# Kernel optimization log

Measured on AMD Instinct MI355X. Metric: run time of the kernel, lower is better.

Reference implementation:

```python
import jax, jax.numpy as jnp
import numpy as np

H = W = 200
A = 9
N = H * W * A  # 360000 anchors
PRE_NMS = 6000   # test mode
POST_NMS = 300
MIN_SIZE = 16.0 / 1000.0
IOU_THR = 0.7


def _conv(x, w, b, pad):
    y = jax.lax.conv_general_dilated(x, w, (1, 1), pad,
                                     dimension_numbers=("NCHW", "OIHW", "NCHW"))
    return y + b[None, :, None, None]


def _nms_keep(boxes, valid, thr):
    # boxes: [PRE_NMS,4] sorted by descending score; valid: [PRE_NMS] bool
    x1, y1, x2, y2 = boxes[:, 0], boxes[:, 1], boxes[:, 2], boxes[:, 3]
    areas = (x2 - x1) * (y2 - y1)
    idx = jnp.arange(boxes.shape[0])

    def body(i, keep):
        xx1 = jnp.maximum(x1[i], x1)
        yy1 = jnp.maximum(y1[i], y1)
        xx2 = jnp.minimum(x2[i], x2)
        yy2 = jnp.minimum(y2[i], y2)
        inter = jnp.clip(xx2 - xx1, 0.0) * jnp.clip(yy2 - yy1, 0.0)
        iou = inter / (areas[i] + areas - inter + 1e-12)
        suppress = (iou > thr) & (idx > i) & keep[i]
        return keep & ~suppress

    return jax.lax.fori_loop(0, boxes.shape[0], body, valid)


def setup_inputs():
    key = jax.random.key(0)
    ks = jax.random.split(key, 6)
    features = jax.random.normal(ks[0], (1, 512, H, W), dtype=jnp.float32)
    # valid anchor boxes (xyxy, normalized)
    c = jax.random.uniform(ks[1], (N, 2), dtype=jnp.float32)
    wh = jax.random.uniform(ks[2], (N, 2), dtype=jnp.float32, minval=0.02, maxval=0.4)
    anchor = jnp.clip(jnp.concatenate([c - wh / 2, c + wh / 2], axis=1), 0.0, 1.0)
    w1 = 0.01 * jax.random.normal(ks[3], (512, 512, 3, 3), dtype=jnp.float32)
    b1 = jnp.zeros((512,), jnp.float32)
    wc = 0.01 * jax.random.normal(ks[4], (2 * A, 512, 1, 1), dtype=jnp.float32)
    bc = jnp.zeros((2 * A,), jnp.float32)
    wl = 0.01 * jax.random.normal(ks[5], (4 * A, 512, 1, 1), dtype=jnp.float32)
    bl = jnp.zeros((4 * A,), jnp.float32)
    return {"features": features, "anchor": anchor,
            "w1": w1, "b1": b1, "wc": wc, "bc": bc, "wl": wl, "bl": bl}


def reference(features, anchor, w1, b1, wc, bc, wl, bl):
    x = jax.nn.relu(_conv(features, w1, b1, ((1, 1), (1, 1))))
    pred_cls = _conv(x, wc, bc, ((0, 0), (0, 0)))
    pred_loc = _conv(x, wl, bl, ((0, 0), (0, 0)))
    pred_cls = jnp.transpose(pred_cls, (0, 2, 3, 1)).reshape(1, -1, 2)  # [1,N,2]
    pred_loc = jnp.transpose(pred_loc, (0, 2, 3, 1)).reshape(1, -1, 4)  # [1,N,4]

    loc = pred_loc[0]
    cls = pred_cls[0]
    # xy_to_cxcy
    a_cxcy = jnp.concatenate([(anchor[:, 2:] + anchor[:, :2]) / 2.0,
                              anchor[:, 2:] - anchor[:, :2]], axis=1)
    # decode
    cxcy = loc[:, :2] * a_cxcy[:, 2:] + a_cxcy[:, :2]
    wh = jnp.exp(loc[:, 2:]) * a_cxcy[:, 2:]
    # cxcy_to_xy + clamp
    roi = jnp.clip(jnp.concatenate([cxcy - wh / 2.0, cxcy + wh / 2.0], axis=1), 0.0, 1.0)

    scores = jax.nn.softmax(cls, axis=-1)[:, 1]
    ws = roi[:, 2] - roi[:, 0]
    hs = roi[:, 3] - roi[:, 1]
    valid = (hs >= MIN_SIZE) & (ws >= MIN_SIZE)
    scores = jnp.where(valid, scores, -1.0)  # filtered boxes sort last

    top_scores, top_idx = jax.lax.top_k(scores, PRE_NMS)
    boxes = roi[top_idx]                      # [PRE_NMS,4]
    valid_top = top_scores >= 0.0

    keep = jax.lax.stop_gradient(_nms_keep(boxes, valid_top, IOU_THR))
    # first POST_NMS kept boxes, in score order; pad with zeros (fixed shape)
    priority = jnp.where(keep, jnp.arange(PRE_NMS), PRE_NMS)
    order = jnp.argsort(priority)[:POST_NMS]
    rois = jnp.where((priority[order] < PRE_NMS)[:, None], boxes[order], 0.0)  # [300,4]
    return pred_cls, pred_loc, rois
```

## Files before the change

kernel.cpp:

```cpp
#include <hip/hip_runtime.h>

typedef unsigned long long u64;
typedef unsigned int u32;
typedef unsigned short ushort_t;

#define HH 200
#define WW 200
#define HWP 40000
#define NANCH 360000
#define PRE 6000
#define POST 300
#define NW 94
#define NBINS 16384
#define KCAP 8192
#define CS 40

typedef __attribute__((ext_vector_type(8))) _Float16 f16x8;
typedef __attribute__((ext_vector_type(4))) float f32x4;

static constexpr size_t X_F    = 0;
static constexpr size_t X_CNT  = 512ULL*HWP + 64;
static constexpr size_t W1B_F  = X_F + X_CNT;
static constexpr size_t WT64_F = W1B_F + 4608ULL*512;
static constexpr size_t B64_F  = WT64_F + 512ULL*64;
static constexpr size_t SC_F   = B64_F + 64;
static constexpr size_t ROI_F  = SC_F + NANCH;
static constexpr size_t BOX_F  = ROI_F + 4ULL*NANCH;
static constexpr size_t FEND_F = BOX_F + 6016ULL*4;
static constexpr size_t HIST_B = ((FEND_F*4 + 255)/256)*256;
static constexpr size_t CTRL_B = HIST_B + NBINS*4;
static constexpr size_t KEY_B  = CTRL_B + 256;
static constexpr size_t SORT_B = KEY_B + (size_t)KCAP*8;
static constexpr size_t VALW_B = SORT_B + 6016ULL*8;
static constexpr size_t MASK_B = ((VALW_B + NW*8 + 255)/256)*256;
static constexpr size_t WS_END = MASK_B + (size_t)PRE*NW*8;

__device__ __forceinline__ u32 fsort(float f) {
  u32 u = __float_as_uint(f);
  return (u & 0x80000000u) ? ~u : (u | 0x80000000u);
}
__device__ __forceinline__ int bucket_of(float s) {
  int b = (int)((s + 1.0f) * 8191.0f);
  return b < 0 ? 0 : (b > 16383 ? 16383 : b);
}
__device__ __forceinline__ ushort_t h_bits(_Float16 h) {
  union { _Float16 h; ushort_t u; } c; c.h = h; return c.u;
}
__device__ __forceinline__ void split_pack(float fA, float fB, u32& w1, u32& w2) {
  _Float16 hA = (_Float16)fA, hB = (_Float16)fB;
  float rA = fA - (float)hA, rB = fB - (float)hB;
  _Float16 cA = (_Float16)(rA * 2048.0f), cB = (_Float16)(rB * 2048.0f);
  w1 = (u32)h_bits(hA) | ((u32)h_bits(hB) << 16);
  w2 = (u32)h_bits(cA) | ((u32)h_bits(cB) << 16);
}

__global__ void pack_w1b(const float* __restrict__ w1, ushort_t* __restrict__ p12) {
  int idx = blockIdx.x*256 + threadIdx.x;
  if (idx >= 512*4608) return;
  int och = idx / 4608, k = idx - (idx/4608)*4608;
  float f = w1[idx];
  _Float16 h1 = (_Float16)f;
  float r = f - (float)h1;
  _Float16 h2 = (_Float16)(r * 2048.0f);
  int ci = k / 9, tap = k - ci*9;
  int chunk = ci >> 5, cil = ci & 31;
  int s = chunk*9 + tap;
  int z = och >> 7, oz = och & 127;
  int wnb = oz >> 6, j = (oz >> 4) & 3, lmm = oz & 15;
  int lg = cil >> 3, e = cil & 7;
  int lane = lg*16 + lmm;
  size_t base = (((size_t)z*144 + s)*2 + wnb)*4 + j;
  p12[base*1024 +       lane*8 + e] = h_bits(h1);
  p12[base*1024 + 512 + lane*8 + e] = h_bits(h2);
}

__global__ void pack_wcl(const float* __restrict__ wc, const float* __restrict__ bc,
                         const float* __restrict__ wl, const float* __restrict__ bl,
                         float* __restrict__ wt, float* __restrict__ b64) {
  int idx = blockIdx.x*256 + threadIdx.x;
  if (idx < 512*64) {
    int ci = idx >> 6, o = idx & 63;
    float v = 0.f;
    if (o < 18) v = wc[o*512 + ci];
    else if (o < 54) v = wl[(o-18)*512 + ci];
    wt[idx] = v;
  } else if (idx < 512*64 + 64) {
    int o = idx - 512*64;
    float v = 0.f;
    if (o < 18) v = bc[o]; else if (o < 54) v = bl[o-18];
    b64[o] = v;
  }
}

__global__ __launch_bounds__(256, 2) void conv3x3_mfma(const float* __restrict__ feat,
    const ushort_t* __restrict__ p12,
    const float* __restrict__ b1, float* __restrict__ xout) {
  __shared__ ushort_t H1[10*18*CS], H2[10*18*CS];
  const int t = threadIdx.x;
  const int x0 = blockIdx.x*16, y0 = blockIdx.y*8;
  const int zi = blockIdx.z;
  const int ob = zi*128;

  const int wave = t >> 6, lane = t & 63;
  const int wm = (wave & 1)*64, wnb = wave >> 1;
  const int lm = lane & 15, lg = lane >> 4;
  const int lyb = wm >> 4;
  const int fragoff = lm*CS + lg*8;

  const int cih = t >> 4;
  const int sxo = t & 15;

  u32* __restrict__ H1u = (u32*)H1;
  u32* __restrict__ H2u = (u32*)H2;

  f32x4 accM[4][4], accC[4][4];
  #pragma unroll
  for (int i = 0; i < 4; ++i)
    #pragma unroll
    for (int j = 0; j < 4; ++j) {
      accM[i][j] = (f32x4){0.f, 0.f, 0.f, 0.f};
      accC[i][j] = (f32x4){0.f, 0.f, 0.f, 0.f};
    }

  const ushort_t* pb = p12 + (size_t)zi*1179648 + (size_t)wnb*4096 + lane*8;
  const float* fbc = feat + (size_t)(2*cih)*HWP;

  for (int c = 0; c < 16; ++c) {
    __syncthreads();
    #pragma unroll
    for (int y = 0; y < 10; ++y) {
      int gy = y0 + y - 1;
      bool yok = (unsigned)gy < 200u;
      int rowoff = gy*200 + x0 - 1;
      {
        int x = sxo;
        int gx = x0 + x - 1;
        bool ok = yok && ((unsigned)gx < 200u);
        int off = ok ? (rowoff + x) : 0;
        float fA = fbc[off], fB = fbc[off + HWP];
        fA = ok ? fA : 0.f;  fB = ok ? fB : 0.f;
        u32 w1v, w2v;  split_pack(fA, fB, w1v, w2v);
        int a = (y*18 + x)*(CS/2) + cih;
        H1u[a] = w1v;  H2u[a] = w2v;
      }
      if (sxo < 2) {
        int x = 16 + sxo;
        int gx = x0 + x - 1;
        bool ok = yok && ((unsigned)gx < 200u);
        int off = ok ? (rowoff + x) : 0;
        float fA = fbc[off], fB = fbc[off + HWP];
        fA = ok ? fA : 0.f;  fB = ok ? fB : 0.f;
        u32 w1v, w2v;  split_pack(fA, fB, w1v, w2v);
        int a = (y*18 + x)*(CS/2) + cih;
        H1u[a] = w1v;  H2u[a] = w2v;
      }
    }
    __syncthreads();
    #pragma unroll 1
    for (int tap = 0; tap < 9; ++tap) {
      const int dy = tap/3, dx = tap - (tap/3)*3;
      f16x8 fb1[4], fb2[4];
      #pragma unroll
      for (int j = 0; j < 4; ++j) {
        fb1[j] = *(const f16x8*)(pb + j*1024);
        fb2[j] = *(const f16x8*)(pb + j*1024 + 512);
      }
      f16x8 fa1[4], fa2[4];
      #pragma unroll
      for (int i = 0; i < 4; ++i) {
        int addr = (lyb + i + dy)*(18*CS) + dx*CS + fragoff;
        fa1[i] = *(const f16x8*)&H1[addr];
        fa2[i] = *(const f16x8*)&H2[addr];
      }
      #pragma unroll
      for (int i = 0; i < 4; ++i)
        #pragma unroll
        for (int j = 0; j < 4; ++j) {
          accM[i][j] = __builtin_amdgcn_mfma_f32_16x16x32_f16(fa1[i], fb1[j], accM[i][j], 0, 0, 0);
          accC[i][j] = __builtin_amdgcn_mfma_f32_16x16x32_f16(fa1[i], fb2[j], accC[i][j], 0, 0, 0);
          accC[i][j] = __builtin_amdgcn_mfma_f32_16x16x32_f16(fa2[i], fb1[j], accC[i][j], 0, 0, 0);
        }
      pb += 8192;
    }
    fbc += 32*HWP;
  }

  #pragma unroll
  for (int i = 0; i < 4; ++i) {
    int prow = wm + i*16 + lg*4;
    #pragma unroll
    for (int j = 0; j < 4; ++j) {
      int o = ob + wnb*64 + j*16 + lm;
      float bias = b1[o];
      #pragma unroll
      for (int r = 0; r < 4; ++r) {
        int p  = prow + r;
        int yy = y0 + (p >> 4), xx = x0 + (p & 15);
        if (xx < WW) {
          float v = accM[i][j][r] + accC[i][j][r] * 4.8828125e-4f + bias;
          xout[(size_t)o*HWP + yy*200 + xx] = fmaxf(v, 0.f);
        }
      }
    }
  }
}

__global__ __launch_bounds__(256, 4) void conv1x1(const float* __restrict__ x,
                                                  const float* __restrict__ wt,
                                                  const float* __restrict__ bias,
                                                  float* __restrict__ out) {
  __shared__ float Xs[16*128];
  __shared__ float Ws[16*64];
  const int t = threadIdx.x;
  const int m0 = blockIdx.x*128;
  float acc[32];
  #pragma unroll
  for (int i = 0; i < 32; ++i) acc[i] = 0.f;
  const int mb = t & 15, nb = t >> 4;
  const int mm = t & 127, hh = t >> 7;
  const int nn = t & 63,  h2 = t >> 6;

  for (int kb = 0; kb < 512; kb += 16) {
    #pragma unroll
    for (int j = 0; j < 8; ++j) {
      int kk = hh + 2*j;
      Xs[kk*128 + mm] = x[(size_t)(kb+kk)*HWP + m0 + mm];
    }
    #pragma unroll
    for (int j = 0; j < 4; ++j) {
      int kk = h2 + 4*j;
      Ws[kk*64 + nn] = wt[(size_t)(kb+kk)*64 + nn];
    }
    __syncthreads();
    #pragma unroll
    for (int kk = 0; kk < 16; ++kk) {
      float av[8], bv[4];
      *(float4*)&av[0] = *(const float4*)&Xs[kk*128 + mb*8];
      *(float4*)&av[4] = *(const float4*)&Xs[kk*128 + mb*8 + 4];
      *(float4*)&bv[0] = *(const float4*)&Ws[kk*64 + nb*4];
      #pragma unroll
      for (int i = 0; i < 8; ++i)
        #pragma unroll
        for (int jj = 0; jj < 4; ++jj)
          acc[i*4+jj] = fmaf(av[i], bv[jj], acc[i*4+jj]);
    }
    __syncthreads();
  }

  #pragma unroll
  for (int jj = 0; jj < 4; ++jj) {
    int o = nb*4 + jj;
    float bv = bias[o];
    #pragma unroll
    for (int i = 0; i < 8; ++i) {
      int mm2 = m0 + mb*8 + i;
      if (mm2 < HWP) {
        float v = acc[i*4+jj] + bv;
        if (o < 18)       out[(size_t)mm2*18 + o] = v;
        else if (o < 54)  out[720000 + (size_t)mm2*36 + (o-18)] = v;
      }
    }
  }
}

__global__ void decode(const float* __restrict__ dout, const float* __restrict__ anchor,
                       float* __restrict__ scores, float4* __restrict__ roi, u32* __restrict__ hist) {
  int n = blockIdx.x*256 + threadIdx.x;
  if (n >= NANCH) return;
  int mq = n / 9;
  int a  = n - mq*9;
  float c0 = dout[(size_t)mq*18 + 2*a];
  float c1 = dout[(size_t)mq*18 + 2*a + 1];
  float score = 1.0f / (1.0f + expf(c0 - c1));
  const float* lp = dout + 720000 + (size_t)mq*36 + 4*a;
  float l0 = lp[0], l1 = lp[1], l2 = lp[2], l3 = lp[3];
  float4 an = ((const float4*)anchor)[n];
  float aw = an.z - an.x, ah = an.w - an.y;
  float acx = (an.x + an.z)*0.5f, acy = (an.y + an.w)*0.5f;
  float cx = l0*aw + acx, cy = l1*ah + acy;
  float bw = expf(l2)*aw, bh = expf(l3)*ah;
  float x1 = fminf(fmaxf(cx - bw*0.5f, 0.f), 1.f);
  float y1 = fminf(fmaxf(cy - bh*0.5f, 0.f), 1.f);
  float x2 = fminf(fmaxf(cx + bw*0.5f, 0.f), 1.f);
  float y2 = fminf(fmaxf(cy + bh*0.5f, 0.f), 1.f);
  bool valid = ((y2 - y1) >= 0.016f) && ((x2 - x1) >= 0.016f);
  float sc = valid ? score : -1.0f;
  scores[n] = sc;
  roi[n] = make_float4(x1, y1, x2, y2);
  atomicAdd(&hist[bucket_of(sc)], 1u);
}

__global__ void scan_hist(const u32* __restrict__ hist, u32* __restrict__ ctrl) {
  __shared__ u32 seg[256];
  int t = threadIdx.x;
  u32 s = 0;
  for (int b = 0; b < 64; ++b) s += hist[t*64 + b];
  seg[t] = s;
  __syncthreads();
  if (t == 0) {
    u32 cum = 0; int B = 0;
    for (int sg = 255; sg >= 0; --sg) {
      if (cum + seg[sg] >= PRE) {
        for (int b = sg*64 + 63; b >= sg*64; --b) {
          cum += hist[b];
          if (cum >= PRE) { B = b; break; }
        }
        break;
      }
      cum += seg[sg];
    }
    ctrl[1] = (u32)B;
  }
}

__global__ void compact(const float* __restrict__ scores, u32* __restrict__ ctrl, u64* __restrict__ keybuf) {
  int n = blockIdx.x*256 + threadIdx.x;
  if (n >= NANCH) return;
  float s = scores[n];
  int B = (int)ctrl[1];
  if (bucket_of(s) >= B) {
    u32 pos = atomicAdd(&ctrl[0], 1u);
    if (pos < KCAP) {
      keybuf[pos] = ((u64)fsort(s) << 32) | (u64)(0xFFFFFFFFu - (u32)n);
    }
  }
}

__global__ __launch_bounds__(1024) void sortk(const u64* __restrict__ keybuf, const u32* __restrict__ ctrl,
                                              u64* __restrict__ sorted) {
  __shared__ u64 s[KCAP];
  int t = threadIdx.x;
  u32 cnt = ctrl[0]; if (cnt > KCAP) cnt = KCAP;
  for (int i = t; i < KCAP; i += 1024) s[i] = (i < (int)cnt) ? keybuf[i] : 0ULL;
  __syncthreads();
  for (int size = 2; size <= KCAP; size <<= 1) {
    for (int stride = size >> 1; stride > 0; stride >>= 1) {
      for (int w = t; w < KCAP/2; w += 1024) {
        int lo = ((w & ~(stride-1)) << 1) | (w & (stride-1));
        int hi = lo + stride;
        bool desc = ((lo & size) == 0);
        u64 a = s[lo], b = s[hi];
        if ((a < b) == desc) { s[lo] = b; s[hi] = a; }
      }
      __syncthreads();
    }
  }
  for (int i = t; i < 6016; i += 1024) sorted[i] = s[i];
}

__global__ void gather_topk(const u64* __restrict__ sorted, const float4* __restrict__ roi,
                            float4* __restrict__ boxes, u64* __restrict__ validw) {
  int i = blockIdx.x*64 + threadIdx.x;
  bool valid = false;
  float4 b = make_float4(0.f, 0.f, 0.f, 0.f);
  if (i < PRE) {
    u64 k = sorted[i];
    if (k) {
      u32 n = 0xFFFFFFFFu - (u32)(k & 0xFFFFFFFFu);
      if (n < NANCH) { b = roi[n]; valid = (k >> 63) != 0; }
    }
  }
  boxes[i] = b;
  u64 bal = __ballot(valid);
  if (threadIdx.x == 0) validw[blockIdx.x] = bal;
}

__global__ void nms_mask(const float4* __restrict__ boxes, u64* __restrict__ mask) {
  int bi = blockIdx.y, bj = blockIdx.x;
  int t = threadIdx.x;
  int i = bi*64 + t;
  if (bj < bi) {
    if (i < PRE) mask[(size_t)i*NW + bj] = 0ULL;
    return;
  }
  __shared__ float4 cb[64];
  int j0 = bj*64;
  cb[t] = boxes[j0 + t];
  __syncthreads();
  if (i >= PRE) return;
  float4 b = boxes[i];
  float area_i = (b.z - b.x) * (b.w - b.y);
  u64 bits = 0;
  #pragma unroll 4
  for (int jj = 0; jj < 64; ++jj) {
    int j = j0 + jj;
    float4 c = cb[jj];
    float xx1 = fmaxf(b.x, c.x), yy1 = fmaxf(b.y, c.y);
    float xx2 = fminf(b.z, c.z), yy2 = fminf(b.w, c.w);
    float inter = fmaxf(xx2 - xx1, 0.f) * fmaxf(yy2 - yy1, 0.f);
    float area_j = (c.z - c.x) * (c.w - c.y);
    float iou = inter / (area_i + area_j - inter + 1e-12f);
    if (iou > 0.7f && j > i) bits |= (1ULL << jj);
  }
  mask[(size_t)i*NW + bj] = bits;
}

__global__ void nms_scan(const u64* __restrict__ mask, const u64* __restrict__ validw,
                         const float* __restrict__ boxes, float* __restrict__ rois) {
  int lane = threadIdx.x;
  u64 r0 = ~validw[lane];
  u64 r1 = (lane < NW-64) ? ~validw[64 + lane] : ~0ULL;
  int kept = 0;
  u64 m0 = mask[lane];
  u64 m1 = (lane < NW-64) ? mask[64 + lane] : 0ULL;
  for (int i = 0; i < PRE; ++i) {
    int wi = i >> 6;
    u64 w0 = __shfl(r0, wi & 63);
    u64 w1 = __shfl(r1, wi & 63);
    u64 wv = (wi < 64) ? w0 : w1;
    if (!((wv >> (i & 63)) & 1ULL)) {
      if (lane < 4) rois[kept*4 + lane] = boxes[(size_t)i*4 + lane];
      kept++;
      if (kept >= POST) break;
      r0 |= m0;
      if (lane < NW-64) r1 |= m1;
    }
    if (i + 1 < PRE) {
      m0 = mask[(size_t)(i+1)*NW + lane];
      m1 = (lane < NW-64) ? mask[(size_t)(i+1)*NW + 64 + lane] : 0ULL;
    }
  }
}

extern "C" void kernel_launch(void* const* d_in, const int* in_sizes, int n_in,
                              void* d_out, int out_size, void* d_ws, size_t ws_size,
                              hipStream_t stream) {
  const float* feat   = (const float*)d_in[0];
  const float* anchor = (const float*)d_in[1];
  const float* w1     = (const float*)d_in[2];
  const float* b1     = (const float*)d_in[3];
  const float* wc     = (const float*)d_in[4];
  const float* bc     = (const float*)d_in[5];
  const float* wl     = (const float*)d_in[6];
  const float* bl     = (const float*)d_in[7];
  float* out = (float*)d_out;
  char*  ws  = (char*)d_ws;
  float* wsf = (float*)d_ws;

  if (ws_size < WS_END) return;

  float*    x      = wsf + X_F;
  ushort_t* p12    = (ushort_t*)(wsf + W1B_F);
  float*    wt64   = wsf + WT64_F;
  float*    b64    = wsf + B64_F;
  float*    scores = wsf + SC_F;
  float4*   roi    = (float4*)(wsf + ROI_F);
  float4*   boxes  = (float4*)(wsf + BOX_F);
  u32* hist   = (u32*)(ws + HIST_B);
  u32* ctrl   = (u32*)(ws + CTRL_B);
  u64* keybuf = (u64*)(ws + KEY_B);
  u64* sorted = (u64*)(ws + SORT_B);
  u64* validw = (u64*)(ws + VALW_B);
  u64* mask   = (u64*)(ws + MASK_B);

  hipMemsetAsync(ws + HIST_B, 0, NBINS*4 + 256, stream);
  hipMemsetAsync(out + 2160000, 0, POST*4*sizeof(float), stream);

  pack_w1b<<<9216, 256, 0, stream>>>(w1, p12);
  pack_wcl<<<129, 256, 0, stream>>>(wc, bc, wl, bl, wt64, b64);
  conv3x3_mfma<<<dim3(13, 25, 4), 256, 0, stream>>>(feat, p12, b1, x);
  conv1x1<<<313, 256, 0, stream>>>(x, wt64, b64, out);
  decode<<<1407, 256, 0, stream>>>(out, anchor, scores, roi, hist);
  scan_hist<<<1, 256, 0, stream>>>(hist, ctrl);
  compact<<<1407, 256, 0, stream>>>(scores, ctrl, keybuf);
  sortk<<<1, 1024, 0, stream>>>(keybuf, ctrl, sorted);
  gather_topk<<<NW, 64, 0, stream>>>(sorted, roi, boxes, validw);
  nms_mask<<<dim3(NW, NW), 64, 0, stream>>>(boxes, mask);
  nms_scan<<<1, 64, 0, stream>>>(mask, validw, (const float*)boxes, out + 2160000);
}
```

Baseline: 1.296 ms.

## Double-buffer conv halo tiles and overlap next-chunk loads with MFMA taps

Adds a second LDS buffer for the input halo tile so the next 32-channel chunk is loaded from global memory and split-packed into fp16 while the current chunk's taps run MFMAs. Loads and writes are staggered across taps 0, 2, 4 and 6 so global latency is hidden behind compute, and one barrier per chunk is removed. In exchange LDS use doubles and register pressure rises from the staged values, which could reduce occupancy at launch_bounds(256,2).

```diff
diff --git a/kernel.cpp b/kernel.cpp
--- a/kernel.cpp
+++ b/kernel.cpp
@@ -52,6 +52,56 @@
   _Float16 cA = (_Float16)(rA * 2048.0f), cB = (_Float16)(rB * 2048.0f);
   w1 = (u32)h_bits(hA) | ((u32)h_bits(hB) << 16);
   w2 = (u32)h_bits(cA) | ((u32)h_bits(cB) << 16);
+}
+
+__device__ __forceinline__ void halo_load(const float* __restrict__ fbn, int y, int y0, int x0,
+                                          int sxo, float& a0, float& b0, float& a1, float& b1) {
+  int gy = y0 + y - 1;
+  bool yok = (unsigned)gy < 200u;
+  int rowoff = gy*200 + x0 - 1;
+  {
+    int gx = x0 + sxo - 1;
+    bool ok = yok && ((unsigned)gx < 200u);
+    int off = ok ? (rowoff + sxo) : 0;
+    float fA = fbn[off], fB = fbn[off + HWP];
+    a0 = ok ? fA : 0.f;  b0 = ok ? fB : 0.f;
+  }
+  if (sxo < 2) {
+    int x = 16 + sxo;
+    int gx = x0 + x - 1;
+    bool ok = yok && ((unsigned)gx < 200u);
+    int off = ok ? (rowoff + x) : 0;
+    float fA = fbn[off], fB = fbn[off + HWP];
+    a1 = ok ? fA : 0.f;  b1 = ok ? fB : 0.f;
+  } else { a1 = 0.f; b1 = 0.f; }
+}
+__device__ __forceinline__ void halo_write(u32* __restrict__ H1u, u32* __restrict__ H2u,
+                                           int y, int sxo, int cih,
+                                           float a0, float b0, float a1, float b1) {
+  u32 w1v, w2v;
+  split_pack(a0, b0, w1v, w2v);
+  H1u[(y*18 + sxo)*(CS/2) + cih] = w1v;
+  H2u[(y*18 + sxo)*(CS/2) + cih] = w2v;
+  if (sxo < 2) {
+    split_pack(a1, b1, w1v, w2v);
+    H1u[(y*18 + 16 + sxo)*(CS/2) + cih] = w1v;
+    H2u[(y*18 + 16 + sxo)*(CS/2) + cih] = w2v;
+  }
+}
+template<int Y0, int NY>
+__device__ __forceinline__ void halo_load_batch(const float* __restrict__ fbn, int y0, int x0,
+                                                int sxo, float* sA, float* sB, float* sA2, float* sB2) {
+  #pragma unroll
+  for (int yy = 0; yy < NY; ++yy)
+    halo_load(fbn, Y0 + yy, y0, x0, sxo, sA[yy], sB[yy], sA2[yy], sB2[yy]);
+}
+template<int Y0, int NY>
+__device__ __forceinline__ void halo_write_batch(u32* __restrict__ H1u, u32* __restrict__ H2u,
+                                                 int sxo, int cih, float* sA, float* sB,
+                                                 float* sA2, float* sB2) {
+  #pragma unroll
+  for (int yy = 0; yy < NY; ++yy)
+    halo_write(H1u, H2u, Y0 + yy, sxo, cih, sA[yy], sB[yy], sA2[yy], sB2[yy]);
 }
 
 __global__ void pack_w1b(const float* __restrict__ w1, ushort_t* __restrict__ p12) {
@@ -95,7 +145,7 @@
 __global__ __launch_bounds__(256, 2) void conv3x3_mfma(const float* __restrict__ feat,
     const ushort_t* __restrict__ p12,
     const float* __restrict__ b1, float* __restrict__ xout) {
-  __shared__ ushort_t H1[10*18*CS], H2[10*18*CS];
+  __shared__ ushort_t H1[2][10*18*CS], H2[2][10*18*CS];
   const int t = threadIdx.x;
   const int x0 = blockIdx.x*16, y0 = blockIdx.y*8;
   const int zi = blockIdx.z;
@@ -109,9 +159,6 @@
 
   const int cih = t >> 4;
   const int sxo = t & 15;
-
-  u32* __restrict__ H1u = (u32*)H1;
-  u32* __restrict__ H2u = (u32*)H2;
 
   f32x4 accM[4][4], accC[4][4];
   #pragma unroll
@@ -123,41 +170,44 @@
     }
 
   const ushort_t* pb = p12 + (size_t)zi*1179648 + (size_t)wnb*4096 + lane*8;
-  const float* fbc = feat + (size_t)(2*cih)*HWP;
+
+  float sA[4], sB[4], sA2[4], sB2[4];
+
+  {
+    const float* fbn = feat + (size_t)(2*cih)*HWP;
+    u32* h1n = (u32*)H1[0];  u32* h2n = (u32*)H2[0];
+    halo_load_batch<0,4>(fbn, y0, x0, sxo, sA, sB, sA2, sB2);
+    halo_write_batch<0,4>(h1n, h2n, sxo, cih, sA, sB, sA2, sB2);
+    halo_load_batch<4,3>(fbn, y0, x0, sxo, sA, sB, sA2, sB2);
+    halo_write_batch<4,3>(h1n, h2n, sxo, cih, sA, sB, sA2, sB2);
+    halo_load_batch<7,3>(fbn, y0, x0, sxo, sA, sB, sA2, sB2);
+    halo_write_batch<7,3>(h1n, h2n, sxo, cih, sA, sB, sA2, sB2);
+  }
 
   for (int c = 0; c < 16; ++c) {
     __syncthreads();
-    #pragma unroll
-    for (int y = 0; y < 10; ++y) {
-      int gy = y0 + y - 1;
-      bool yok = (unsigned)gy < 200u;
-      int rowoff = gy*200 + x0 - 1;
-      {
-        int x = sxo;
-        int gx = x0 + x - 1;
-        bool ok = yok && ((unsigned)gx < 200u);
-        int off = ok ? (rowoff + x) : 0;
-        float fA = fbc[off], fB = fbc[off + HWP];
-        fA = ok ? fA : 0.f;  fB = ok ? fB : 0.f;
-        u32 w1v, w2v;  split_pack(fA, fB, w1v, w2v);
-        int a = (y*18 + x)*(CS/2) + cih;
-        H1u[a] = w1v;  H2u[a] = w2v;
-      }
-      if (sxo < 2) {
-        int x = 16 + sxo;
-        int gx = x0 + x - 1;
-        bool ok = yok && ((unsigned)gx < 200u);
-        int off = ok ? (rowoff + x) : 0;
-        float fA = fbc[off], fB = fbc[off + HWP];
-        fA = ok ? fA : 0.f;  fB = ok ? fB : 0.f;
-        u32 w1v, w2v;  split_pack(fA, fB, w1v, w2v);
-        int a = (y*18 + x)*(CS/2) + cih;
-        H1u[a] = w1v;  H2u[a] = w2v;
-      }
-    }
-    __syncthreads();
+    const ushort_t* h1c = H1[c & 1];
+    const ushort_t* h2c = H2[c & 1];
+    u32* h1n = (u32*)H1[(c + 1) & 1];
+    u32* h2n = (u32*)H2[(c + 1) & 1];
+    const float* fbn = feat + (size_t)(2*cih)*HWP + (size_t)(c + 1)*32*HWP;
+    const bool more = (c < 15);
+
     #pragma unroll 1
     for (int tap = 0; tap < 9; ++tap) {
+      if (more) {
+        if (tap == 0) {
+          halo_load_batch<0,4>(fbn, y0, x0, sxo, sA, sB, sA2, sB2);
+        } else if (tap == 2) {
+          halo_write_batch<0,4>(h1n, h2n, sxo, cih, sA, sB, sA2, sB2);
+          halo_load_batch<4,3>(fbn, y0, x0, sxo, sA, sB, sA2, sB2);
+        } else if (tap == 4) {
+          halo_write_batch<4,3>(h1n, h2n, sxo, cih, sA, sB, sA2, sB2);
+          halo_load_batch<7,3>(fbn, y0, x0, sxo, sA, sB, sA2, sB2);
+        } else if (tap == 6) {
+          halo_write_batch<7,3>(h1n, h2n, sxo, cih, sA, sB, sA2, sB2);
+        }
+      }
       const int dy = tap/3, dx = tap - (tap/3)*3;
       f16x8 fb1[4], fb2[4];
       #pragma unroll
@@ -169,8 +219,8 @@
       #pragma unroll
       for (int i = 0; i < 4; ++i) {
         int addr = (lyb + i + dy)*(18*CS) + dx*CS + fragoff;
-        fa1[i] = *(const f16x8*)&H1[addr];
-        fa2[i] = *(const f16x8*)&H2[addr];
+        fa1[i] = *(const f16x8*)&h1c[addr];
+        fa2[i] = *(const f16x8*)&h2c[addr];
       }
       #pragma unroll
       for (int i = 0; i < 4; ++i)
@@ -182,7 +232,6 @@
         }
       pb += 8192;
     }
-    fbc += 32*HWP;
   }
 
   #pragma unroll
```

Result: slower. 1.696 ms (+30.9%).
